# Kernel tuning notes

Hardware: AMD Instinct MI355X
Metric: run time of the kernel (lower is better)

## Reference

```python
import jax, jax.numpy as jnp
import numpy as np
from jax import lax

STRIDE = 4
SCALES = (32.0, 64.0, 128.0)
RATIOS = (0.5, 1.0, 2.0)
PRE_NMS = 6000          # pre_nms_top_n['testing']
POST_NMS = 1000         # post_nms_top_n['testing']
NMS_THRESH = 0.7
MIN_SIZE = 1.0


def make_anchors(fh, fw):
    # 9 base anchors per cell (3 scales x 3 ratios), xyxy centered at cell centers.
    base = []
    for s in SCALES:
        for r in RATIOS:
            w = s * np.sqrt(1.0 / r)
            h = s * np.sqrt(r)
            base.append([-w / 2, -h / 2, w / 2, h / 2])
    base = np.asarray(base, np.float32)                      # [9,4]
    xs = (np.arange(fw, dtype=np.float32) + 0.5) * STRIDE
    ys = (np.arange(fh, dtype=np.float32) + 0.5) * STRIDE
    cx, cy = np.meshgrid(xs, ys)                             # [fh,fw]
    shifts = np.stack([cx, cy, cx, cy], -1)[:, :, None, :]   # [fh,fw,1,4]
    return jnp.asarray((shifts + base[None, None]).reshape(-1, 4))  # [fh*fw*9,4]


def conv(x, w, b):
    y = lax.conv_general_dilated(x, w, (1, 1), 'SAME',
                                 dimension_numbers=('NCHW', 'OIHW', 'NCHW'))
    return y + b[None, :, None, None]


def decode(anchors, deltas):
    wa = anchors[:, 2] - anchors[:, 0]
    ha = anchors[:, 3] - anchors[:, 1]
    cxa = anchors[:, 0] + 0.5 * wa
    cya = anchors[:, 1] + 0.5 * ha
    cx = deltas[:, 0] * wa + cxa
    cy = deltas[:, 1] * ha + cya
    w = jnp.exp(deltas[:, 2]) * wa
    h = jnp.exp(deltas[:, 3]) * ha
    return jnp.stack([cx - 0.5 * w, cy - 0.5 * h, cx + 0.5 * w, cy + 0.5 * h], -1)


def pairwise_iou(a, b):
    area_a = (a[:, 2] - a[:, 0]) * (a[:, 3] - a[:, 1])
    area_b = (b[:, 2] - b[:, 0]) * (b[:, 3] - b[:, 1])
    lt = jnp.maximum(a[:, None, :2], b[None, :, :2])
    rb = jnp.minimum(a[:, None, 2:], b[None, :, 2:])
    wh = jnp.clip(rb - lt, 0.0)
    inter = wh[..., 0] * wh[..., 1]
    return inter / (area_a[:, None] + area_b[None, :] - inter + 1e-9)


def nms_keep(boxes, valid, thresh):
    # boxes already sorted by score descending; greedy suppression.
    n = boxes.shape[0]
    iou = pairwise_iou(boxes, boxes)  # [n,n]
    def body(i, keep):
        suppressed = jnp.any((iou[i] > thresh) & keep)
        return keep.at[i].set(valid[i] & ~suppressed)
    return lax.fori_loop(0, n, body, jnp.zeros(n, bool))


def rpn_forward(feature, w1, b1, w_cls, b_cls, w_reg, b_reg, image_h, image_w,
                detach_for_proposal=True):
    fh, fw = feature.shape[2], feature.shape[3]
    x = jax.nn.relu(conv(feature, w1, b1))
    conf = conv(x, w_cls, b_cls).transpose(0, 2, 3, 1).reshape(-1)        # [N]
    offsets = conv(x, w_reg, b_reg).transpose(0, 2, 3, 1).reshape(-1, 4)  # [N,4]
    if detach_for_proposal:  # original detaches before create_proposal
        conf = lax.stop_gradient(conf)
        offsets = lax.stop_gradient(offsets)
    anchors = make_anchors(fh, fw)

    pre_n = min(PRE_NMS, conf.shape[0])
    scores, idx = lax.top_k(conf, pre_n)
    props = decode(anchors[idx], offsets[idx])
    # process_box: clip to image, drop boxes smaller than min_size (mask form)
    props = jnp.stack([jnp.clip(props[:, 0], 0.0, float(image_w)),
                       jnp.clip(props[:, 1], 0.0, float(image_h)),
                       jnp.clip(props[:, 2], 0.0, float(image_w)),
                       jnp.clip(props[:, 3], 0.0, float(image_h))], -1)
    valid = ((props[:, 2] - props[:, 0]) >= MIN_SIZE) & \
            ((props[:, 3] - props[:, 1]) >= MIN_SIZE)

    keep = nms_keep(lax.stop_gradient(props), valid, NMS_THRESH)
    # compact first POST_NMS kept boxes into a fixed-shape output (zero padded)
    rank = jnp.cumsum(keep) - 1
    dest = jnp.where(keep & (rank < POST_NMS), rank, POST_NMS)
    out = jnp.zeros((POST_NMS + 1, 4), props.dtype).at[dest].set(props)[:POST_NMS]
    return out


def setup_inputs() -> dict:
    key = jax.random.key(0)
    ks = jax.random.split(key, 4)
    return {
        'feature': jax.random.normal(ks[0], (1, 256, 200, 272), jnp.float32),
        'w1': jax.random.normal(ks[1], (256, 256, 3, 3), jnp.float32) * 0.02,
        'b1': jnp.zeros((256,), jnp.float32),
        'w_cls': jax.random.normal(ks[2], (9, 256, 1, 1), jnp.float32) * 0.02,
        'b_cls': jnp.zeros((9,), jnp.float32),
        'w_reg': jax.random.normal(ks[3], (36, 256, 1, 1), jnp.float32) * 0.01,
        'b_reg': jnp.zeros((36,), jnp.float32),
        'image_h': 800,
        'image_w': 1088,
    }


def reference(feature, w1, b1, w_cls, b_cls, w_reg, b_reg, image_h, image_w):
    return rpn_forward(feature, w1, b1, w_cls, b_cls, w_reg, b_reg,
                       image_h, image_w, detach_for_proposal=True)
```

## Files before the change

### kernel.cpp

```cpp
#include <hip/hip_runtime.h>
#include <hip/hip_bf16.h>
#include <math.h>

#define H_ 200
#define W_ 272
#define C_ 256
#define HW 54400
#define NANCH 489600
#define PRE_N 6000
#define POST_N 1000
#define NWORDS 94
#define CHUNK_W 2720

#define X_OFF       0ull
#define CONF_OFF    55705600ull
#define HIST1_OFF   57664000ull
#define HIST2_OFF   57926144ull
#define SCAL_OFF    58188288ull
#define SEL_OFF     58188544ull
#define TOPIDX_OFF  58254080ull
#define BOXES_OFF   58278080ull
#define VALID_OFF   58374080ull
#define MASK_OFF    58398080ull
#define W1R_OFF     62910080ull
#define WCR_OFF     65269376ull

__device__ __forceinline__ unsigned fkey(float fv) {
    unsigned u = __float_as_uint(fv);
    return (u & 0x80000000u) ? ~u : (u | 0x80000000u);
}

__global__ __launch_bounds__(256) void k_init(const float* __restrict__ w1,
                                              const float* __restrict__ wcls,
                                              unsigned* __restrict__ hist1,
                                              float* __restrict__ w1r,
                                              float* __restrict__ wcr) {
    int e = blockIdx.x * 256 + threadIdx.x;
    if (e < 131136) hist1[e] = 0u;
    int e1 = e - 131136;
    if (e1 >= 0 && e1 < 589824) {
        int oc = e1 / 2304; int rem = e1 % 2304; int ic = rem / 9; int k = rem % 9;
        int wg = oc >> 3, o = oc & 7;
        w1r[(((size_t)wg * 256 + ic) * 9 + k) * 8 + o] = w1[e1];
    } else if (e1 >= 589824 && e1 < 589824 + 2304) {
        int e2 = e1 - 589824; int a = e2 / 256; int c = e2 % 256;
        wcr[c * 9 + a] = wcls[e2];
    }
}

__global__ __launch_bounds__(256) void k_conv1(const float* __restrict__ f,
                                               const float* __restrict__ w1r,
                                               const float* __restrict__ b1,
                                               float* __restrict__ xo) {
    __shared__ __align__(16) float sI[2][2880];
    int tid = threadIdx.x;
    int lane = tid & 63;
    int wgl = __builtin_amdgcn_readfirstlane(tid >> 6);
    int xg = lane & 7;
    int yg = lane >> 3;
    int X0 = blockIdx.x * 32;
    int Y0 = blockIdx.y * 8;
    int wg = blockIdx.z * 4 + wgl;
    int y = Y0 + yg;
    int xbase = X0 + xg * 4;

    int off[11]; int lds[11]; bool ok[11];
#pragma unroll
    for (int it = 0; it < 11; it++) {
        int l = tid + it * 256;
        int ci = l / 340; int r = l - ci * 340; int ry = r / 34; int rx = r - ry * 34;
        int gx = X0 - 1 + rx, gy = Y0 - 1 + ry;
        ok[it] = (l < CHUNK_W) && gx >= 0 && gx < W_ && gy >= 0 && gy < H_;
        off[it] = ci * HW + gy * W_ + gx;
        lds[it] = (ci * 10 + ry) * 36 + rx;
    }
    float rbuf[11];
#pragma unroll
    for (int it = 0; it < 11; it++)
        rbuf[it] = ok[it] ? f[off[it]] : 0.f;
#pragma unroll
    for (int it = 0; it < 11; it++)
        if (tid + it * 256 < CHUNK_W) sI[0][lds[it]] = rbuf[it];
    __syncthreads();

    float acc[8][4];
#pragma unroll
    for (int o = 0; o < 8; o++)
#pragma unroll
        for (int i = 0; i < 4; i++) acc[o][i] = 0.f;

    const float* wbase = w1r + (size_t)wg * 256 * 72;

    int cur = 0;
    for (int ic0 = 0; ic0 < 256; ic0 += 8) {
        if (ic0 < 248) {
            const float* fn = f + (size_t)(ic0 + 8) * HW;
#pragma unroll
            for (int it = 0; it < 11; it++)
                rbuf[it] = ok[it] ? fn[off[it]] : 0.f;
        }
        const float* sbuf = sI[cur];
        for (int ci = 0; ci < 8; ci++) {
            const float* wp = wbase + (size_t)(ic0 + ci) * 72;
#pragma unroll
            for (int ky = 0; ky < 3; ky++) {
                const float* irow = &sbuf[(ci * 10 + yg + ky) * 36 + xg * 4];
                float4 va = *(const float4*)irow;
                float2 vb = *(const float2*)(irow + 4);
                float in[6] = {va.x, va.y, va.z, va.w, vb.x, vb.y};
                const float* wrow = wp + ky * 24;
#pragma unroll
                for (int kx = 0; kx < 3; kx++) {
#pragma unroll
                    for (int o = 0; o < 8; o++) {
                        float w = wrow[kx * 8 + o];
#pragma unroll
                        for (int i = 0; i < 4; i++)
                            acc[o][i] = fmaf(w, in[i + kx], acc[o][i]);
                    }
                }
            }
        }
        if (ic0 < 248) {
#pragma unroll
            for (int it = 0; it < 11; it++)
                if (tid + it * 256 < CHUNK_W) sI[cur ^ 1][lds[it]] = rbuf[it];
        }
        __syncthreads();
        cur ^= 1;
    }
#pragma unroll
    for (int o = 0; o < 8; o++) {
        int oc = wg * 8 + o;
        float bv = b1[oc];
        float* orow = xo + (size_t)oc * HW + y * W_ + xbase;
        float v0 = fmaxf(acc[o][0] + bv, 0.f), v1 = fmaxf(acc[o][1] + bv, 0.f);
        float v2 = fmaxf(acc[o][2] + bv, 0.f), v3 = fmaxf(acc[o][3] + bv, 0.f);
        if (xbase + 3 < W_) {
            *(float4*)orow = make_float4(v0, v1, v2, v3);
        } else {
            float vv[4] = {v0, v1, v2, v3};
            for (int i = 0; i < 4; i++)
                if (xbase + i < W_) orow[i] = vv[i];
        }
    }
}

__global__ __launch_bounds__(256) void k_cls(const float* __restrict__ x,
                                             const float* __restrict__ wcr,
                                             const float* __restrict__ bc,
                                             float* __restrict__ conf,
                                             unsigned* __restrict__ hist) {
    int p = blockIdx.x * 256 + threadIdx.x;
    if (p >= HW) return;
    float acc[9];
#pragma unroll
    for (int a = 0; a < 9; a++) acc[a] = 0.f;
    for (int c = 0; c < 256; c++) {
        float xv = x[c * HW + p];
        const float* wp = wcr + c * 9;
#pragma unroll
        for (int a = 0; a < 9; a++) acc[a] = fmaf(wp[a], xv, acc[a]);
    }
#pragma unroll
    for (int a = 0; a < 9; a++) {
        float v = acc[a] + bc[a];
        conf[p * 9 + a] = v;
        atomicAdd(&hist[fkey(v) >> 16], 1u);
    }
}

__global__ __launch_bounds__(256) void k_hist2(const float* __restrict__ conf,
                                               const unsigned* __restrict__ scal, unsigned* hist) {
    int n = blockIdx.x * 256 + threadIdx.x;
    if (n >= NANCH) return;
    unsigned key = fkey(conf[n]);
    if ((key >> 16) == scal[0]) atomicAdd(&hist[key & 0xFFFFu], 1u);
}

__global__ __launch_bounds__(1024) void k_scan(const unsigned* __restrict__ hist,
                                               unsigned* scal, int mode) {
    __shared__ unsigned ssum[1024];
    int t = threadIdx.x;
    unsigned target = 6000u - (mode ? scal[1] : 0u);
    int base = 65535 - t * 64;
    unsigned s = 0;
    for (int k = 0; k < 64; k++) s += hist[base - k];
    ssum[t] = s;
    __syncthreads();
    for (int off = 1; off < 1024; off <<= 1) {
        unsigned v = (t >= off) ? ssum[t - off] : 0u;
        __syncthreads();
        ssum[t] += v;
        __syncthreads();
    }
    unsigned incl = ssum[t], excl = incl - s;
    if (excl < target && target <= incl) {
        unsigned run = excl;
        for (int k = 0; k < 64; k++) {
            unsigned c = hist[base - k];
            if (run + c >= target) { scal[2 * mode] = (unsigned)(base - k); scal[2 * mode + 1] = run; break; }
            run += c;
        }
    }
}

__global__ __launch_bounds__(256) void k_gather(const float* __restrict__ conf,
                                                unsigned* scal, unsigned long long* sel) {
    int n = blockIdx.x * 256 + threadIdx.x;
    if (n >= NANCH) return;
    unsigned B1 = scal[0], cnt1 = scal[1], B2 = scal[2], cnt2 = scal[3];
    unsigned T = (B1 << 16) | B2;
    unsigned key = fkey(conf[n]);
    if (key < T) return;
    unsigned long long kk = ((unsigned long long)(~key) << 32) | (unsigned)n;
    if (key > T) {
        unsigned pos = atomicAdd(&scal[4], 1u);
        if (pos < 8192u) sel[pos] = kk;
    } else {
        unsigned pos = cnt1 + cnt2 + atomicAdd(&scal[5], 1u);
        if (pos < 8192u) sel[pos] = kk;
    }
}

__global__ __launch_bounds__(256) void k_rank(const unsigned* __restrict__ scal,
                                              const unsigned long long* __restrict__ sel,
                                              unsigned* __restrict__ topidx) {
    __shared__ unsigned long long tile[2048];
    unsigned G = scal[1] + scal[3];
    unsigned filled = G + scal[5];
    if (filled > 8192u) filled = 8192u;
    int i = blockIdx.x * 256 + threadIdx.x;
    unsigned long long mykey = (i < (int)filled) ? sel[i] : 0xFFFFFFFFFFFFFFFFull;
    int rank = 0;
    for (int t0 = 0; t0 < 8192; t0 += 2048) {
        __syncthreads();
        for (int l = threadIdx.x; l < 2048; l += 256) {
            int j = t0 + l;
            tile[l] = (j < (int)filled) ? sel[j] : 0xFFFFFFFFFFFFFFFFull;
        }
        __syncthreads();
        for (int l = 0; l < 2048; l += 4) {
            ulonglong2 p = *(const ulonglong2*)&tile[l];
            ulonglong2 q = *(const ulonglong2*)&tile[l + 2];
            rank += (p.x < mykey) + (p.y < mykey) + (q.x < mykey) + (q.y < mykey);
        }
    }
    if (i < (int)filled && rank < PRE_N)
        topidx[rank] = (unsigned)(mykey & 0xFFFFFFFFull);
}

__global__ __launch_bounds__(64) void k_prop(const float* __restrict__ x,
                                             const float* __restrict__ wreg,
                                             const float* __restrict__ breg,
                                             const unsigned* __restrict__ topidx,
                                             const int* __restrict__ imh, const int* __restrict__ imw,
                                             float* __restrict__ boxes, int* __restrict__ valid) {
    int r = blockIdx.x;
    int lane = threadIdx.x;
    unsigned n = topidx[r];
    int a = (int)(n % 9u); int p = (int)(n / 9u);
    const float* wr = wreg + (4 * a) * 256;
    float s0 = 0, s1 = 0, s2 = 0, s3 = 0;
    for (int c = lane; c < 256; c += 64) {
        float xv = x[c * HW + p];
        s0 = fmaf(wr[c], xv, s0);
        s1 = fmaf(wr[256 + c], xv, s1);
        s2 = fmaf(wr[512 + c], xv, s2);
        s3 = fmaf(wr[768 + c], xv, s3);
    }
#pragma unroll
    for (int off = 32; off >= 1; off >>= 1) {
        s0 += __shfl_down(s0, off);
        s1 += __shfl_down(s1, off);
        s2 += __shfl_down(s2, off);
        s3 += __shfl_down(s3, off);
    }
    if (lane == 0) {
        float dx = s0 + breg[4 * a], dy = s1 + breg[4 * a + 1];
        float dw = s2 + breg[4 * a + 2], dh = s3 + breg[4 * a + 3];
        int wi = p % W_, hi = p / W_;
        const double SC[3] = {32.0, 64.0, 128.0};
        const double RT[3] = {0.5, 1.0, 2.0};
        double sd = SC[a / 3], rd = RT[a % 3];
        double wb = sd * sqrt(1.0 / rd), hb = sd * sqrt(rd);
        float bx1 = (float)(-wb * 0.5), by1 = (float)(-hb * 0.5);
        float bx2 = (float)(wb * 0.5),  by2 = (float)(hb * 0.5);
        float cxs = ((float)wi + 0.5f) * 4.0f, cys = ((float)hi + 0.5f) * 4.0f;
        float x1a = cxs + bx1, y1a = cys + by1, x2a = cxs + bx2, y2a = cys + by2;
        float wa = x2a - x1a, ha = y2a - y1a;
        float cxa = x1a + 0.5f * wa, cya = y1a + 0.5f * ha;
        float cx = dx * wa + cxa, cy = dy * ha + cya;
        float ww = expf(dw) * wa, hh = expf(dh) * ha;
        float X1 = cx - 0.5f * ww, Y1 = cy - 0.5f * hh;
        float X2 = cx + 0.5f * ww, Y2 = cy + 0.5f * hh;
        float Wf = (float)(*imw), Hf = (float)(*imh);
        X1 = fminf(fmaxf(X1, 0.f), Wf); Y1 = fminf(fmaxf(Y1, 0.f), Hf);
        X2 = fminf(fmaxf(X2, 0.f), Wf); Y2 = fminf(fmaxf(Y2, 0.f), Hf);
        boxes[4 * r] = X1; boxes[4 * r + 1] = Y1; boxes[4 * r + 2] = X2; boxes[4 * r + 3] = Y2;
        valid[r] = ((X2 - X1) >= 1.0f && (Y2 - Y1) >= 1.0f) ? 1 : 0;
    }
}

__global__ __launch_bounds__(256) void k_mask(const float* __restrict__ boxes,
                                              unsigned long long* __restrict__ mask) {
    __shared__ float jb[256];
    int jw = blockIdx.x;
    int i = blockIdx.y * 256 + threadIdx.x;
    {
        int idx = jw * 256 + threadIdx.x;
        jb[threadIdx.x] = (idx < PRE_N * 4) ? boxes[idx] : 0.f;
    }
    __syncthreads();
    if (i >= PRE_N) return;
    float ax1 = boxes[4 * i], ay1 = boxes[4 * i + 1], ax2 = boxes[4 * i + 2], ay2 = boxes[4 * i + 3];
    float aarea = (ax2 - ax1) * (ay2 - ay1);
    unsigned long long m = 0;
    int jbase = jw * 64;
    for (int b = 0; b < 64; b++) {
        int j = jbase + b;
        if (j <= i || j >= PRE_N) continue;
        float bx1 = jb[4 * b], by1 = jb[4 * b + 1], bx2 = jb[4 * b + 2], by2 = jb[4 * b + 3];
        float barea = (bx2 - bx1) * (by2 - by1);
        float xx1 = fmaxf(ax1, bx1), yy1 = fmaxf(ay1, by1);
        float xx2 = fminf(ax2, bx2), yy2 = fminf(ay2, by2);
        float w = fmaxf(xx2 - xx1, 0.f), h = fmaxf(yy2 - yy1, 0.f);
        float inter = w * h;
        float iou = inter / (aarea + barea - inter + 1e-9f);
        if (iou > 0.7f) m |= (1ull << b);
    }
    mask[(size_t)i * NWORDS + jw] = m;
}

__global__ __launch_bounds__(128) void k_scan_nms(const unsigned long long* __restrict__ mask,
                                                  const int* __restrict__ valid,
                                                  const float* __restrict__ boxes,
                                                  float* __restrict__ out) {
    __shared__ unsigned long long diag[NWORDS][64];
    __shared__ unsigned long long removed[NWORDS];
    __shared__ unsigned long long validw[NWORDS];
    __shared__ int keepList[POST_N];
    __shared__ int cnt;
    __shared__ unsigned long long keptbits;
    int t = threadIdx.x;
    if (t < NWORDS) { removed[t] = 0ull; validw[t] = 0ull; }
    if (t == 0) cnt = 0;
    __syncthreads();
    for (int l = t; l < NWORDS * 64; l += 128) {
        int w = l >> 6, b = l & 63;
        int i = w * 64 + b;
        diag[w][b] = (i < PRE_N) ? mask[(size_t)i * NWORDS + w] : 0ull;
    }
    for (int i = t; i < PRE_N; i += 128)
        if (valid[i]) atomicOr(&validw[i >> 6], 1ull << (i & 63));
    __syncthreads();
    for (int w = 0; w < NWORDS; w++) {
        unsigned long long candw = validw[w] & ~removed[w];
        if (!candw) continue;
        if (t == 0) {
            unsigned long long cand = candw;
            unsigned long long kb = 0ull;
            int c = cnt;
            while (cand && c < POST_N) {
                int b = __ffsll((unsigned long long)cand) - 1;
                keepList[c++] = w * 64 + b;
                kb |= 1ull << b;
                cand &= ~(1ull << b);
                cand &= ~diag[w][b];
            }
            cnt = c; keptbits = kb;
        }
        __syncthreads();
        if (cnt >= POST_N) break;
        unsigned long long kb = keptbits;
        if (kb) {
            for (int w2 = w + 1 + t; w2 < NWORDS; w2 += 128) {
                unsigned long long acc2 = removed[w2];
                unsigned long long tt = kb;
                while (tt) {
                    int b = __ffsll((unsigned long long)tt) - 1;
                    tt &= tt - 1;
                    acc2 |= mask[(size_t)(w * 64 + b) * NWORDS + w2];
                }
                removed[w2] = acc2;
            }
        }
        __syncthreads();
    }
    __syncthreads();
    int c = cnt;
    for (int e = t; e < POST_N * 4; e += 128) {
        int r = e >> 2;
        out[e] = (r < c) ? boxes[4 * keepList[r] + (e & 3)] : 0.f;
    }
}

extern "C" void kernel_launch(void* const* d_in, const int* in_sizes, int n_in,
                              void* d_out, int out_size, void* d_ws, size_t ws_size,
                              hipStream_t stream) {
    const float* feature = (const float*)d_in[0];
    const float* w1   = (const float*)d_in[1];
    const float* b1   = (const float*)d_in[2];
    const float* wcls = (const float*)d_in[3];
    const float* bcls = (const float*)d_in[4];
    const float* wreg = (const float*)d_in[5];
    const float* breg = (const float*)d_in[6];
    const int* imh = (const int*)d_in[7];
    const int* imw = (const int*)d_in[8];

    char* ws = (char*)d_ws;
    float* xbuf  = (float*)(ws + X_OFF);
    float* conf  = (float*)(ws + CONF_OFF);
    unsigned* hist1 = (unsigned*)(ws + HIST1_OFF);
    unsigned* hist2 = (unsigned*)(ws + HIST2_OFF);
    unsigned* scal  = (unsigned*)(ws + SCAL_OFF);
    unsigned long long* sel = (unsigned long long*)(ws + SEL_OFF);
    unsigned* topidx = (unsigned*)(ws + TOPIDX_OFF);
    float* boxes = (float*)(ws + BOXES_OFF);
    int* valid   = (int*)(ws + VALID_OFF);
    unsigned long long* mask = (unsigned long long*)(ws + MASK_OFF);
    float* w1r = (float*)(ws + W1R_OFF);
    float* wcr = (float*)(ws + WCR_OFF);
    float* outF = (float*)d_out;

    hipLaunchKernelGGL(k_init,   dim3(2826), dim3(256), 0, stream, w1, wcls, hist1, w1r, wcr);
    hipLaunchKernelGGL(k_conv1,  dim3(9, 25, 8), dim3(256), 0, stream, feature, w1r, b1, xbuf);
    hipLaunchKernelGGL(k_cls,    dim3(213),  dim3(256), 0, stream, xbuf, wcr, bcls, conf, hist1);
    hipLaunchKernelGGL(k_scan,   dim3(1),    dim3(1024), 0, stream, hist1, scal, 0);
    hipLaunchKernelGGL(k_hist2,  dim3(1913), dim3(256), 0, stream, conf, scal, hist2);
    hipLaunchKernelGGL(k_scan,   dim3(1),    dim3(1024), 0, stream, hist2, scal, 1);
    hipLaunchKernelGGL(k_gather, dim3(1913), dim3(256), 0, stream, conf, scal, sel);
    hipLaunchKernelGGL(k_rank,   dim3(32),   dim3(256), 0, stream, scal, sel, topidx);
    hipLaunchKernelGGL(k_prop,   dim3(PRE_N), dim3(64), 0, stream, xbuf, wreg, breg, topidx, imh, imw, boxes, valid);
    hipLaunchKernelGGL(k_mask,   dim3(NWORDS, 24), dim3(256), 0, stream, boxes, mask);
    hipLaunchKernelGGL(k_scan_nms, dim3(1), dim3(128), 0, stream, mask, valid, boxes, outF);
}
```

Baseline: 1.594 ms.

## Fuse post-conv pipeline into one cooperative persistent kernel with grid syncs

Replaces the nine post-convolution launches (cls head, two histogram/scan passes, gather, rank, proposal decode, IoU mask, NMS scan) with a single cooperative kernel of 256 blocks that separates the stages with grid.sync. The aim is to remove per-launch overhead and idle gaps between the many small serial kernels. In exchange, the wide stages (cls head and the full-anchor passes) now run on only 256 blocks with grid-stride loops, giving less occupancy than before. The single-block scans and NMS also leave the rest of the grid waiting at the barriers.

```diff
diff --git a/kernel.cpp b/kernel.cpp
--- a/kernel.cpp
+++ b/kernel.cpp
@@ -1,6 +1,9 @@
 #include <hip/hip_runtime.h>
 #include <hip/hip_bf16.h>
+#include <hip/hip_cooperative_groups.h>
 #include <math.h>
+
+namespace cg = cooperative_groups;
 
 #define H_ 200
 #define W_ 272
@@ -146,252 +149,299 @@
     }
 }
 
-__global__ __launch_bounds__(256) void k_cls(const float* __restrict__ x,
-                                             const float* __restrict__ wcr,
-                                             const float* __restrict__ bc,
-                                             float* __restrict__ conf,
-                                             unsigned* __restrict__ hist) {
-    int p = blockIdx.x * 256 + threadIdx.x;
-    if (p >= HW) return;
-    float acc[9];
-#pragma unroll
-    for (int a = 0; a < 9; a++) acc[a] = 0.f;
-    for (int c = 0; c < 256; c++) {
-        float xv = x[c * HW + p];
-        const float* wp = wcr + c * 9;
-#pragma unroll
-        for (int a = 0; a < 9; a++) acc[a] = fmaf(wp[a], xv, acc[a]);
-    }
-#pragma unroll
-    for (int a = 0; a < 9; a++) {
-        float v = acc[a] + bc[a];
-        conf[p * 9 + a] = v;
-        atomicAdd(&hist[fkey(v) >> 16], 1u);
-    }
-}
-
-__global__ __launch_bounds__(256) void k_hist2(const float* __restrict__ conf,
-                                               const unsigned* __restrict__ scal, unsigned* hist) {
-    int n = blockIdx.x * 256 + threadIdx.x;
-    if (n >= NANCH) return;
-    unsigned key = fkey(conf[n]);
-    if ((key >> 16) == scal[0]) atomicAdd(&hist[key & 0xFFFFu], 1u);
-}
-
-__global__ __launch_bounds__(1024) void k_scan(const unsigned* __restrict__ hist,
-                                               unsigned* scal, int mode) {
-    __shared__ unsigned ssum[1024];
+union SharedU {
+    unsigned ssum[256];
+    unsigned long long tile[2048];
+    float jb[256];
+    struct {
+        unsigned long long diag[NWORDS][64];
+        unsigned long long removed[NWORDS];
+        unsigned long long validw[NWORDS];
+        int keepList[POST_N];
+        int cnt;
+        unsigned long long keptbits;
+    } nms;
+};
+
+__global__ __launch_bounds__(256) void k_post(const float* __restrict__ x,
+                                              const float* __restrict__ wcr,
+                                              const float* __restrict__ bc,
+                                              float* __restrict__ conf,
+                                              unsigned* __restrict__ hist1,
+                                              unsigned* __restrict__ hist2,
+                                              unsigned* __restrict__ scal,
+                                              unsigned long long* __restrict__ sel,
+                                              unsigned* __restrict__ topidx,
+                                              const float* __restrict__ wreg,
+                                              const float* __restrict__ breg,
+                                              const int* __restrict__ imh,
+                                              const int* __restrict__ imw,
+                                              float* __restrict__ boxes,
+                                              int* __restrict__ validA,
+                                              unsigned long long* __restrict__ mask,
+                                              float* __restrict__ out) {
+    __shared__ SharedU su;
+    cg::grid_group grid = cg::this_grid();
     int t = threadIdx.x;
-    unsigned target = 6000u - (mode ? scal[1] : 0u);
-    int base = 65535 - t * 64;
-    unsigned s = 0;
-    for (int k = 0; k < 64; k++) s += hist[base - k];
-    ssum[t] = s;
-    __syncthreads();
-    for (int off = 1; off < 1024; off <<= 1) {
-        unsigned v = (t >= off) ? ssum[t - off] : 0u;
-        __syncthreads();
-        ssum[t] += v;
-        __syncthreads();
-    }
-    unsigned incl = ssum[t], excl = incl - s;
-    if (excl < target && target <= incl) {
-        unsigned run = excl;
-        for (int k = 0; k < 64; k++) {
-            unsigned c = hist[base - k];
-            if (run + c >= target) { scal[2 * mode] = (unsigned)(base - k); scal[2 * mode + 1] = run; break; }
-            run += c;
-        }
-    }
-}
-
-__global__ __launch_bounds__(256) void k_gather(const float* __restrict__ conf,
-                                                unsigned* scal, unsigned long long* sel) {
-    int n = blockIdx.x * 256 + threadIdx.x;
-    if (n >= NANCH) return;
-    unsigned B1 = scal[0], cnt1 = scal[1], B2 = scal[2], cnt2 = scal[3];
-    unsigned T = (B1 << 16) | B2;
-    unsigned key = fkey(conf[n]);
-    if (key < T) return;
-    unsigned long long kk = ((unsigned long long)(~key) << 32) | (unsigned)n;
-    if (key > T) {
-        unsigned pos = atomicAdd(&scal[4], 1u);
-        if (pos < 8192u) sel[pos] = kk;
-    } else {
-        unsigned pos = cnt1 + cnt2 + atomicAdd(&scal[5], 1u);
-        if (pos < 8192u) sel[pos] = kk;
-    }
-}
-
-__global__ __launch_bounds__(256) void k_rank(const unsigned* __restrict__ scal,
-                                              const unsigned long long* __restrict__ sel,
-                                              unsigned* __restrict__ topidx) {
-    __shared__ unsigned long long tile[2048];
-    unsigned G = scal[1] + scal[3];
-    unsigned filled = G + scal[5];
-    if (filled > 8192u) filled = 8192u;
-    int i = blockIdx.x * 256 + threadIdx.x;
-    unsigned long long mykey = (i < (int)filled) ? sel[i] : 0xFFFFFFFFFFFFFFFFull;
-    int rank = 0;
-    for (int t0 = 0; t0 < 8192; t0 += 2048) {
-        __syncthreads();
-        for (int l = threadIdx.x; l < 2048; l += 256) {
-            int j = t0 + l;
-            tile[l] = (j < (int)filled) ? sel[j] : 0xFFFFFFFFFFFFFFFFull;
-        }
-        __syncthreads();
-        for (int l = 0; l < 2048; l += 4) {
-            ulonglong2 p = *(const ulonglong2*)&tile[l];
-            ulonglong2 q = *(const ulonglong2*)&tile[l + 2];
-            rank += (p.x < mykey) + (p.y < mykey) + (q.x < mykey) + (q.y < mykey);
-        }
-    }
-    if (i < (int)filled && rank < PRE_N)
-        topidx[rank] = (unsigned)(mykey & 0xFFFFFFFFull);
-}
-
-__global__ __launch_bounds__(64) void k_prop(const float* __restrict__ x,
-                                             const float* __restrict__ wreg,
-                                             const float* __restrict__ breg,
-                                             const unsigned* __restrict__ topidx,
-                                             const int* __restrict__ imh, const int* __restrict__ imw,
-                                             float* __restrict__ boxes, int* __restrict__ valid) {
-    int r = blockIdx.x;
-    int lane = threadIdx.x;
-    unsigned n = topidx[r];
-    int a = (int)(n % 9u); int p = (int)(n / 9u);
-    const float* wr = wreg + (4 * a) * 256;
-    float s0 = 0, s1 = 0, s2 = 0, s3 = 0;
-    for (int c = lane; c < 256; c += 64) {
-        float xv = x[c * HW + p];
-        s0 = fmaf(wr[c], xv, s0);
-        s1 = fmaf(wr[256 + c], xv, s1);
-        s2 = fmaf(wr[512 + c], xv, s2);
-        s3 = fmaf(wr[768 + c], xv, s3);
-    }
-#pragma unroll
-    for (int off = 32; off >= 1; off >>= 1) {
-        s0 += __shfl_down(s0, off);
-        s1 += __shfl_down(s1, off);
-        s2 += __shfl_down(s2, off);
-        s3 += __shfl_down(s3, off);
-    }
-    if (lane == 0) {
-        float dx = s0 + breg[4 * a], dy = s1 + breg[4 * a + 1];
-        float dw = s2 + breg[4 * a + 2], dh = s3 + breg[4 * a + 3];
-        int wi = p % W_, hi = p / W_;
-        const double SC[3] = {32.0, 64.0, 128.0};
-        const double RT[3] = {0.5, 1.0, 2.0};
-        double sd = SC[a / 3], rd = RT[a % 3];
-        double wb = sd * sqrt(1.0 / rd), hb = sd * sqrt(rd);
-        float bx1 = (float)(-wb * 0.5), by1 = (float)(-hb * 0.5);
-        float bx2 = (float)(wb * 0.5),  by2 = (float)(hb * 0.5);
-        float cxs = ((float)wi + 0.5f) * 4.0f, cys = ((float)hi + 0.5f) * 4.0f;
-        float x1a = cxs + bx1, y1a = cys + by1, x2a = cxs + bx2, y2a = cys + by2;
-        float wa = x2a - x1a, ha = y2a - y1a;
-        float cxa = x1a + 0.5f * wa, cya = y1a + 0.5f * ha;
-        float cx = dx * wa + cxa, cy = dy * ha + cya;
-        float ww = expf(dw) * wa, hh = expf(dh) * ha;
-        float X1 = cx - 0.5f * ww, Y1 = cy - 0.5f * hh;
-        float X2 = cx + 0.5f * ww, Y2 = cy + 0.5f * hh;
-        float Wf = (float)(*imw), Hf = (float)(*imh);
-        X1 = fminf(fmaxf(X1, 0.f), Wf); Y1 = fminf(fmaxf(Y1, 0.f), Hf);
-        X2 = fminf(fmaxf(X2, 0.f), Wf); Y2 = fminf(fmaxf(Y2, 0.f), Hf);
-        boxes[4 * r] = X1; boxes[4 * r + 1] = Y1; boxes[4 * r + 2] = X2; boxes[4 * r + 3] = Y2;
-        valid[r] = ((X2 - X1) >= 1.0f && (Y2 - Y1) >= 1.0f) ? 1 : 0;
-    }
-}
-
-__global__ __launch_bounds__(256) void k_mask(const float* __restrict__ boxes,
-                                              unsigned long long* __restrict__ mask) {
-    __shared__ float jb[256];
-    int jw = blockIdx.x;
-    int i = blockIdx.y * 256 + threadIdx.x;
+    int gid = blockIdx.x * 256 + t;
+
+    for (int p = gid; p < HW; p += 65536) {
+        float acc[9];
+#pragma unroll
+        for (int a = 0; a < 9; a++) acc[a] = 0.f;
+        for (int c = 0; c < 256; c++) {
+            float xv = x[c * HW + p];
+            const float* wp = wcr + c * 9;
+#pragma unroll
+            for (int a = 0; a < 9; a++) acc[a] = fmaf(wp[a], xv, acc[a]);
+        }
+#pragma unroll
+        for (int a = 0; a < 9; a++) {
+            float v = acc[a] + bc[a];
+            conf[p * 9 + a] = v;
+            atomicAdd(&hist1[fkey(v) >> 16], 1u);
+        }
+    }
+    grid.sync();
+
+    if (blockIdx.x == 0) {
+        unsigned target = 6000u;
+        int base = 65535 - t * 256;
+        unsigned s = 0;
+        const uint4* hp = (const uint4*)(hist1 + (base - 255));
+        for (int k = 0; k < 64; k++) { uint4 v = hp[k]; s += v.x + v.y + v.z + v.w; }
+        su.ssum[t] = s;
+        __syncthreads();
+        for (int o = 1; o < 256; o <<= 1) {
+            unsigned v = (t >= o) ? su.ssum[t - o] : 0u;
+            __syncthreads();
+            su.ssum[t] += v;
+            __syncthreads();
+        }
+        unsigned incl = su.ssum[t], excl = incl - s;
+        if (excl < target && target <= incl) {
+            unsigned run = excl;
+            for (int k = 0; k < 256; k++) {
+                unsigned c = hist1[base - k];
+                if (run + c >= target) { scal[0] = (unsigned)(base - k); scal[1] = run; break; }
+                run += c;
+            }
+        }
+    }
+    grid.sync();
+
     {
-        int idx = jw * 256 + threadIdx.x;
-        jb[threadIdx.x] = (idx < PRE_N * 4) ? boxes[idx] : 0.f;
-    }
-    __syncthreads();
-    if (i >= PRE_N) return;
-    float ax1 = boxes[4 * i], ay1 = boxes[4 * i + 1], ax2 = boxes[4 * i + 2], ay2 = boxes[4 * i + 3];
-    float aarea = (ax2 - ax1) * (ay2 - ay1);
-    unsigned long long m = 0;
-    int jbase = jw * 64;
-    for (int b = 0; b < 64; b++) {
-        int j = jbase + b;
-        if (j <= i || j >= PRE_N) continue;
-        float bx1 = jb[4 * b], by1 = jb[4 * b + 1], bx2 = jb[4 * b + 2], by2 = jb[4 * b + 3];
-        float barea = (bx2 - bx1) * (by2 - by1);
-        float xx1 = fmaxf(ax1, bx1), yy1 = fmaxf(ay1, by1);
-        float xx2 = fminf(ax2, bx2), yy2 = fminf(ay2, by2);
-        float w = fmaxf(xx2 - xx1, 0.f), h = fmaxf(yy2 - yy1, 0.f);
-        float inter = w * h;
-        float iou = inter / (aarea + barea - inter + 1e-9f);
-        if (iou > 0.7f) m |= (1ull << b);
-    }
-    mask[(size_t)i * NWORDS + jw] = m;
-}
-
-__global__ __launch_bounds__(128) void k_scan_nms(const unsigned long long* __restrict__ mask,
-                                                  const int* __restrict__ valid,
-                                                  const float* __restrict__ boxes,
-                                                  float* __restrict__ out) {
-    __shared__ unsigned long long diag[NWORDS][64];
-    __shared__ unsigned long long removed[NWORDS];
-    __shared__ unsigned long long validw[NWORDS];
-    __shared__ int keepList[POST_N];
-    __shared__ int cnt;
-    __shared__ unsigned long long keptbits;
-    int t = threadIdx.x;
-    if (t < NWORDS) { removed[t] = 0ull; validw[t] = 0ull; }
-    if (t == 0) cnt = 0;
-    __syncthreads();
-    for (int l = t; l < NWORDS * 64; l += 128) {
-        int w = l >> 6, b = l & 63;
-        int i = w * 64 + b;
-        diag[w][b] = (i < PRE_N) ? mask[(size_t)i * NWORDS + w] : 0ull;
-    }
-    for (int i = t; i < PRE_N; i += 128)
-        if (valid[i]) atomicOr(&validw[i >> 6], 1ull << (i & 63));
-    __syncthreads();
-    for (int w = 0; w < NWORDS; w++) {
-        unsigned long long candw = validw[w] & ~removed[w];
-        if (!candw) continue;
-        if (t == 0) {
-            unsigned long long cand = candw;
-            unsigned long long kb = 0ull;
-            int c = cnt;
-            while (cand && c < POST_N) {
-                int b = __ffsll((unsigned long long)cand) - 1;
-                keepList[c++] = w * 64 + b;
-                kb |= 1ull << b;
-                cand &= ~(1ull << b);
-                cand &= ~diag[w][b];
-            }
-            cnt = c; keptbits = kb;
-        }
-        __syncthreads();
-        if (cnt >= POST_N) break;
-        unsigned long long kb = keptbits;
-        if (kb) {
-            for (int w2 = w + 1 + t; w2 < NWORDS; w2 += 128) {
-                unsigned long long acc2 = removed[w2];
-                unsigned long long tt = kb;
-                while (tt) {
-                    int b = __ffsll((unsigned long long)tt) - 1;
-                    tt &= tt - 1;
-                    acc2 |= mask[(size_t)(w * 64 + b) * NWORDS + w2];
+        unsigned B1 = scal[0];
+        for (int n = gid; n < NANCH; n += 65536) {
+            unsigned key = fkey(conf[n]);
+            if ((key >> 16) == B1) atomicAdd(&hist2[key & 0xFFFFu], 1u);
+        }
+    }
+    grid.sync();
+
+    if (blockIdx.x == 0) {
+        unsigned target = 6000u - scal[1];
+        int base = 65535 - t * 256;
+        unsigned s = 0;
+        const uint4* hp = (const uint4*)(hist2 + (base - 255));
+        for (int k = 0; k < 64; k++) { uint4 v = hp[k]; s += v.x + v.y + v.z + v.w; }
+        su.ssum[t] = s;
+        __syncthreads();
+        for (int o = 1; o < 256; o <<= 1) {
+            unsigned v = (t >= o) ? su.ssum[t - o] : 0u;
+            __syncthreads();
+            su.ssum[t] += v;
+            __syncthreads();
+        }
+        unsigned incl = su.ssum[t], excl = incl - s;
+        if (excl < target && target <= incl) {
+            unsigned run = excl;
+            for (int k = 0; k < 256; k++) {
+                unsigned c = hist2[base - k];
+                if (run + c >= target) { scal[2] = (unsigned)(base - k); scal[3] = run; break; }
+                run += c;
+            }
+        }
+    }
+    grid.sync();
+
+    {
+        unsigned B1 = scal[0], cnt1 = scal[1], B2 = scal[2], cnt2 = scal[3];
+        unsigned T = (B1 << 16) | B2;
+        for (int n = gid; n < NANCH; n += 65536) {
+            unsigned key = fkey(conf[n]);
+            if (key < T) continue;
+            unsigned long long kk = ((unsigned long long)(~key) << 32) | (unsigned)n;
+            if (key > T) {
+                unsigned pos = atomicAdd(&scal[4], 1u);
+                if (pos < 8192u) sel[pos] = kk;
+            } else {
+                unsigned pos = cnt1 + cnt2 + atomicAdd(&scal[5], 1u);
+                if (pos < 8192u) sel[pos] = kk;
+            }
+        }
+    }
+    grid.sync();
+
+    {
+        unsigned G = scal[1] + scal[3];
+        unsigned filled = G + scal[5];
+        if (filled > 8192u) filled = 8192u;
+        if (blockIdx.x < 32) {
+            int i = blockIdx.x * 256 + t;
+            unsigned long long mykey = (i < (int)filled) ? sel[i] : 0xFFFFFFFFFFFFFFFFull;
+            int rank = 0;
+            for (int t0 = 0; t0 < 8192; t0 += 2048) {
+                __syncthreads();
+                for (int l = t; l < 2048; l += 256) {
+                    int j = t0 + l;
+                    su.tile[l] = (j < (int)filled) ? sel[j] : 0xFFFFFFFFFFFFFFFFull;
                 }
-                removed[w2] = acc2;
-            }
-        }
-        __syncthreads();
-    }
-    __syncthreads();
-    int c = cnt;
-    for (int e = t; e < POST_N * 4; e += 128) {
-        int r = e >> 2;
-        out[e] = (r < c) ? boxes[4 * keepList[r] + (e & 3)] : 0.f;
+                __syncthreads();
+                for (int l = 0; l < 2048; l += 4) {
+                    ulonglong2 p = *(const ulonglong2*)&su.tile[l];
+                    ulonglong2 q = *(const ulonglong2*)&su.tile[l + 2];
+                    rank += (p.x < mykey) + (p.y < mykey) + (q.x < mykey) + (q.y < mykey);
+                }
+            }
+            if (i < (int)filled && rank < PRE_N)
+                topidx[rank] = (unsigned)(mykey & 0xFFFFFFFFull);
+        }
+    }
+    grid.sync();
+
+    {
+        int wave = blockIdx.x * 4 + (t >> 6);
+        int lane = t & 63;
+        for (int r = wave; r < PRE_N; r += 1024) {
+            unsigned n = topidx[r];
+            int a = (int)(n % 9u); int p = (int)(n / 9u);
+            const float* wr = wreg + (4 * a) * 256;
+            float s0 = 0, s1 = 0, s2 = 0, s3 = 0;
+            for (int c = lane; c < 256; c += 64) {
+                float xv = x[c * HW + p];
+                s0 = fmaf(wr[c], xv, s0);
+                s1 = fmaf(wr[256 + c], xv, s1);
+                s2 = fmaf(wr[512 + c], xv, s2);
+                s3 = fmaf(wr[768 + c], xv, s3);
+            }
+#pragma unroll
+            for (int o = 32; o >= 1; o >>= 1) {
+                s0 += __shfl_down(s0, o);
+                s1 += __shfl_down(s1, o);
+                s2 += __shfl_down(s2, o);
+                s3 += __shfl_down(s3, o);
+            }
+            if (lane == 0) {
+                float dx = s0 + breg[4 * a], dy = s1 + breg[4 * a + 1];
+                float dw = s2 + breg[4 * a + 2], dh = s3 + breg[4 * a + 3];
+                int wi = p % W_, hi = p / W_;
+                const double SC[3] = {32.0, 64.0, 128.0};
+                const double RT[3] = {0.5, 1.0, 2.0};
+                double sd = SC[a / 3], rd = RT[a % 3];
+                double wb = sd * sqrt(1.0 / rd), hb = sd * sqrt(rd);
+                float bx1 = (float)(-wb * 0.5), by1 = (float)(-hb * 0.5);
+                float bx2 = (float)(wb * 0.5),  by2 = (float)(hb * 0.5);
+                float cxs = ((float)wi + 0.5f) * 4.0f, cys = ((float)hi + 0.5f) * 4.0f;
+                float x1a = cxs + bx1, y1a = cys + by1, x2a = cxs + bx2, y2a = cys + by2;
+                float wa = x2a - x1a, ha = y2a - y1a;
+                float cxa = x1a + 0.5f * wa, cya = y1a + 0.5f * ha;
+                float cx = dx * wa + cxa, cy = dy * ha + cya;
+                float ww = expf(dw) * wa, hh = expf(dh) * ha;
+                float X1 = cx - 0.5f * ww, Y1 = cy - 0.5f * hh;
+                float X2 = cx + 0.5f * ww, Y2 = cy + 0.5f * hh;
+                float Wf = (float)(*imw), Hf = (float)(*imh);
+                X1 = fminf(fmaxf(X1, 0.f), Wf); Y1 = fminf(fmaxf(Y1, 0.f), Hf);
+                X2 = fminf(fmaxf(X2, 0.f), Wf); Y2 = fminf(fmaxf(Y2, 0.f), Hf);
+                boxes[4 * r] = X1; boxes[4 * r + 1] = Y1; boxes[4 * r + 2] = X2; boxes[4 * r + 3] = Y2;
+                validA[r] = ((X2 - X1) >= 1.0f && (Y2 - Y1) >= 1.0f) ? 1 : 0;
+            }
+        }
+    }
+    grid.sync();
+
+    for (int tile = blockIdx.x; tile < NWORDS * 24; tile += 256) {
+        int jw = tile / 24, ib = tile - jw * 24;
+        __syncthreads();
+        {
+            int idx = jw * 256 + t;
+            su.jb[t] = (idx < PRE_N * 4) ? boxes[idx] : 0.f;
+        }
+        __syncthreads();
+        int i = ib * 256 + t;
+        if (i < PRE_N) {
+            float ax1 = boxes[4 * i], ay1 = boxes[4 * i + 1], ax2 = boxes[4 * i + 2], ay2 = boxes[4 * i + 3];
+            float aarea = (ax2 - ax1) * (ay2 - ay1);
+            unsigned long long m = 0;
+            int jbase = jw * 64;
+            for (int b = 0; b < 64; b++) {
+                int j = jbase + b;
+                if (j <= i || j >= PRE_N) continue;
+                float bx1 = su.jb[4 * b], by1 = su.jb[4 * b + 1], bx2 = su.jb[4 * b + 2], by2 = su.jb[4 * b + 3];
+                float barea = (bx2 - bx1) * (by2 - by1);
+                float xx1 = fmaxf(ax1, bx1), yy1 = fmaxf(ay1, by1);
+                float xx2 = fminf(ax2, bx2), yy2 = fminf(ay2, by2);
+                float w = fmaxf(xx2 - xx1, 0.f), h = fmaxf(yy2 - yy1, 0.f);
+                float inter = w * h;
+                float iou = inter / (aarea + barea - inter + 1e-9f);
+                if (iou > 0.7f) m |= (1ull << b);
+            }
+            mask[(size_t)i * NWORDS + jw] = m;
+        }
+    }
+    grid.sync();
+
+    if (blockIdx.x == 0) {
+        if (t < NWORDS) { su.nms.removed[t] = 0ull; su.nms.validw[t] = 0ull; }
+        if (t == 0) su.nms.cnt = 0;
+        __syncthreads();
+        for (int l = t; l < NWORDS * 64; l += 256) {
+            int w = l >> 6, b = l & 63;
+            int i = w * 64 + b;
+            su.nms.diag[w][b] = (i < PRE_N) ? mask[(size_t)i * NWORDS + w] : 0ull;
+        }
+        for (int i = t; i < PRE_N; i += 256)
+            if (validA[i]) atomicOr(&su.nms.validw[i >> 6], 1ull << (i & 63));
+        __syncthreads();
+        for (int w = 0; w < NWORDS; w++) {
+            unsigned long long candw = su.nms.validw[w] & ~su.nms.removed[w];
+            if (!candw) continue;
+            if (t == 0) {
+                unsigned long long cand = candw;
+                unsigned long long kb = 0ull;
+                int c = su.nms.cnt;
+                while (cand && c < POST_N) {
+                    int b = __ffsll((unsigned long long)cand) - 1;
+                    su.nms.keepList[c++] = w * 64 + b;
+                    kb |= 1ull << b;
+                    cand &= ~(1ull << b);
+                    cand &= ~su.nms.diag[w][b];
+                }
+                su.nms.cnt = c; su.nms.keptbits = kb;
+            }
+            __syncthreads();
+            if (su.nms.cnt >= POST_N) break;
+            unsigned long long kb = su.nms.keptbits;
+            if (kb) {
+                for (int w2 = w + 1 + t; w2 < NWORDS; w2 += 256) {
+                    unsigned long long acc2 = su.nms.removed[w2];
+                    unsigned long long tt = kb;
+                    while (tt) {
+                        int b = __ffsll((unsigned long long)tt) - 1;
+                        tt &= tt - 1;
+                        acc2 |= mask[(size_t)(w * 64 + b) * NWORDS + w2];
+                    }
+                    su.nms.removed[w2] = acc2;
+                }
+            }
+            __syncthreads();
+        }
+        __syncthreads();
+        int c = su.nms.cnt;
+        for (int e = t; e < POST_N * 4; e += 256) {
+            int r = e >> 2;
+            out[e] = (r < c) ? boxes[4 * su.nms.keepList[r] + (e & 3)] : 0.f;
+        }
     }
 }
 
@@ -423,15 +473,13 @@
     float* wcr = (float*)(ws + WCR_OFF);
     float* outF = (float*)d_out;
 
-    hipLaunchKernelGGL(k_init,   dim3(2826), dim3(256), 0, stream, w1, wcls, hist1, w1r, wcr);
-    hipLaunchKernelGGL(k_conv1,  dim3(9, 25, 8), dim3(256), 0, stream, feature, w1r, b1, xbuf);
-    hipLaunchKernelGGL(k_cls,    dim3(213),  dim3(256), 0, stream, xbuf, wcr, bcls, conf, hist1);
-    hipLaunchKernelGGL(k_scan,   dim3(1),    dim3(1024), 0, stream, hist1, scal, 0);
-    hipLaunchKernelGGL(k_hist2,  dim3(1913), dim3(256), 0, stream, conf, scal, hist2);
-    hipLaunchKernelGGL(k_scan,   dim3(1),    dim3(1024), 0, stream, hist2, scal, 1);
-    hipLaunchKernelGGL(k_gather, dim3(1913), dim3(256), 0, stream, conf, scal, sel);
-    hipLaunchKernelGGL(k_rank,   dim3(32),   dim3(256), 0, stream, scal, sel, topidx);
-    hipLaunchKernelGGL(k_prop,   dim3(PRE_N), dim3(64), 0, stream, xbuf, wreg, breg, topidx, imh, imw, boxes, valid);
-    hipLaunchKernelGGL(k_mask,   dim3(NWORDS, 24), dim3(256), 0, stream, boxes, mask);
-    hipLaunchKernelGGL(k_scan_nms, dim3(1), dim3(128), 0, stream, mask, valid, boxes, outF);
+    hipLaunchKernelGGL(k_init,  dim3(2826), dim3(256), 0, stream, w1, wcls, hist1, w1r, wcr);
+    hipLaunchKernelGGL(k_conv1, dim3(9, 25, 8), dim3(256), 0, stream, feature, w1r, b1, xbuf);
+
+    void* args[] = {(void*)&xbuf, (void*)&wcr, (void*)&bcls, (void*)&conf,
+                    (void*)&hist1, (void*)&hist2, (void*)&scal, (void*)&sel,
+                    (void*)&topidx, (void*)&wreg, (void*)&breg, (void*)&imh,
+                    (void*)&imw, (void*)&boxes, (void*)&valid, (void*)&mask,
+                    (void*)&outF};
+    hipLaunchCooperativeKernel((void*)k_post, dim3(256), dim3(256), args, 0, stream);
 }
```

New measurement: 1.826 ms. 14.6% more time.

## Fold init into conv, drop second histogram pass, and use single-level radix select

Applied to the files above, without the earlier changes.

Removes the separate init kernel. Zeroing of the histogram, scalars and selection buffer, plus the cls-weight transpose, now happen at the start of the conv kernel. The conv kernel reads the original OIHW weights directly instead of a pre-transposed copy. The two-level radix select becomes one level: candidates in the threshold bucket go into a larger selection buffer and are ranked by brute-force compare, with early exit past the filled count. This removes a launch, the second histogram pass and a scan. The trade-offs are more scattered scalar weight loads inside the conv inner loop and more rank work when the tie bucket is large. Selection may be wrong if the tie bucket overflows the buffer capacity.

```diff
diff --git a/kernel.cpp b/kernel.cpp
--- a/kernel.cpp
+++ b/kernel.cpp
@@ -11,18 +11,17 @@
 #define POST_N 1000
 #define NWORDS 94
 #define CHUNK_W 2720
+#define SELCAP 16384
 
 #define X_OFF       0ull
 #define CONF_OFF    55705600ull
 #define HIST1_OFF   57664000ull
-#define HIST2_OFF   57926144ull
+#define SEL_OFF     57926144ull
 #define SCAL_OFF    58188288ull
-#define SEL_OFF     58188544ull
 #define TOPIDX_OFF  58254080ull
 #define BOXES_OFF   58278080ull
 #define VALID_OFF   58374080ull
 #define MASK_OFF    58398080ull
-#define W1R_OFF     62910080ull
 #define WCR_OFF     65269376ull
 
 __device__ __forceinline__ unsigned fkey(float fv) {
@@ -30,30 +29,30 @@
     return (u & 0x80000000u) ? ~u : (u | 0x80000000u);
 }
 
-__global__ __launch_bounds__(256) void k_init(const float* __restrict__ w1,
-                                              const float* __restrict__ wcls,
-                                              unsigned* __restrict__ hist1,
-                                              float* __restrict__ w1r,
-                                              float* __restrict__ wcr) {
-    int e = blockIdx.x * 256 + threadIdx.x;
-    if (e < 131136) hist1[e] = 0u;
-    int e1 = e - 131136;
-    if (e1 >= 0 && e1 < 589824) {
-        int oc = e1 / 2304; int rem = e1 % 2304; int ic = rem / 9; int k = rem % 9;
-        int wg = oc >> 3, o = oc & 7;
-        w1r[(((size_t)wg * 256 + ic) * 9 + k) * 8 + o] = w1[e1];
-    } else if (e1 >= 589824 && e1 < 589824 + 2304) {
-        int e2 = e1 - 589824; int a = e2 / 256; int c = e2 % 256;
-        wcr[c * 9 + a] = wcls[e2];
-    }
-}
-
 __global__ __launch_bounds__(256) void k_conv1(const float* __restrict__ f,
-                                               const float* __restrict__ w1r,
+                                               const float* __restrict__ w1,
                                                const float* __restrict__ b1,
-                                               float* __restrict__ xo) {
+                                               float* __restrict__ xo,
+                                               unsigned* __restrict__ hist1,
+                                               unsigned* __restrict__ scal,
+                                               unsigned long long* __restrict__ sel,
+                                               const float* __restrict__ wcls,
+                                               float* __restrict__ wcr) {
     __shared__ __align__(16) float sI[2][2880];
     int tid = threadIdx.x;
+    int fb = blockIdx.x + 9 * (blockIdx.y + 25 * blockIdx.z);
+    {
+        int g = fb * 256 + tid;
+        if (g < 65536) hist1[g] = 0u;
+        else if (g < 65600) scal[g - 65536] = 0u;
+        else if (g < 98368) ((unsigned*)sel)[g - 65600] = 0xFFFFFFFFu;
+    }
+    if (fb == 0) {
+        for (int e = tid; e < 2304; e += 256) {
+            int a = e / 256, c = e % 256;
+            wcr[c * 9 + a] = wcls[e];
+        }
+    }
     int lane = tid & 63;
     int wgl = __builtin_amdgcn_readfirstlane(tid >> 6);
     int xg = lane & 7;
@@ -89,7 +88,7 @@
 #pragma unroll
         for (int i = 0; i < 4; i++) acc[o][i] = 0.f;
 
-    const float* wbase = w1r + (size_t)wg * 256 * 72;
+    const float* wbase = w1 + (size_t)(wg * 8) * 2304;
 
     int cur = 0;
     for (int ic0 = 0; ic0 < 256; ic0 += 8) {
@@ -101,19 +100,18 @@
         }
         const float* sbuf = sI[cur];
         for (int ci = 0; ci < 8; ci++) {
-            const float* wp = wbase + (size_t)(ic0 + ci) * 72;
+            const float* wci = wbase + (ic0 + ci) * 9;
 #pragma unroll
             for (int ky = 0; ky < 3; ky++) {
                 const float* irow = &sbuf[(ci * 10 + yg + ky) * 36 + xg * 4];
                 float4 va = *(const float4*)irow;
                 float2 vb = *(const float2*)(irow + 4);
                 float in[6] = {va.x, va.y, va.z, va.w, vb.x, vb.y};
-                const float* wrow = wp + ky * 24;
 #pragma unroll
                 for (int kx = 0; kx < 3; kx++) {
 #pragma unroll
                     for (int o = 0; o < 8; o++) {
-                        float w = wrow[kx * 8 + o];
+                        float w = wci[o * 2304 + ky * 3 + kx];
 #pragma unroll
                         for (int i = 0; i < 4; i++)
                             acc[o][i] = fmaf(w, in[i + kx], acc[o][i]);
@@ -170,22 +168,17 @@
     }
 }
 
-__global__ __launch_bounds__(256) void k_hist2(const float* __restrict__ conf,
-                                               const unsigned* __restrict__ scal, unsigned* hist) {
-    int n = blockIdx.x * 256 + threadIdx.x;
-    if (n >= NANCH) return;
-    unsigned key = fkey(conf[n]);
-    if ((key >> 16) == scal[0]) atomicAdd(&hist[key & 0xFFFFu], 1u);
-}
-
 __global__ __launch_bounds__(1024) void k_scan(const unsigned* __restrict__ hist,
-                                               unsigned* scal, int mode) {
+                                               unsigned* scal) {
     __shared__ unsigned ssum[1024];
     int t = threadIdx.x;
-    unsigned target = 6000u - (mode ? scal[1] : 0u);
     int base = 65535 - t * 64;
     unsigned s = 0;
-    for (int k = 0; k < 64; k++) s += hist[base - k];
+    {
+        const uint4* hp = (const uint4*)(hist + (base - 63));
+#pragma unroll
+        for (int k = 0; k < 16; k++) { uint4 v = hp[k]; s += v.x + v.y + v.z + v.w; }
+    }
     ssum[t] = s;
     __syncthreads();
     for (int off = 1; off < 1024; off <<= 1) {
@@ -195,12 +188,22 @@
         __syncthreads();
     }
     unsigned incl = ssum[t], excl = incl - s;
-    if (excl < target && target <= incl) {
+    if (excl < 6000u && 6000u <= incl) {
         unsigned run = excl;
-        for (int k = 0; k < 64; k++) {
-            unsigned c = hist[base - k];
-            if (run + c >= target) { scal[2 * mode] = (unsigned)(base - k); scal[2 * mode + 1] = run; break; }
-            run += c;
+        bool found = false;
+        for (int pass = 0; pass < 2 && !found; pass++) {
+            unsigned c32[32];
+#pragma unroll
+            for (int j = 0; j < 32; j++) c32[j] = hist[base - (pass * 32 + j)];
+            for (int j = 0; j < 32; j++) {
+                if (run + c32[j] >= 6000u) {
+                    scal[0] = (unsigned)(base - (pass * 32 + j));
+                    scal[1] = run;
+                    found = true;
+                    break;
+                }
+                run += c32[j];
+            }
         }
     }
 }
@@ -209,17 +212,17 @@
                                                 unsigned* scal, unsigned long long* sel) {
     int n = blockIdx.x * 256 + threadIdx.x;
     if (n >= NANCH) return;
-    unsigned B1 = scal[0], cnt1 = scal[1], B2 = scal[2], cnt2 = scal[3];
-    unsigned T = (B1 << 16) | B2;
+    unsigned B1 = scal[0], cnt1 = scal[1];
     unsigned key = fkey(conf[n]);
-    if (key < T) return;
+    unsigned pre = key >> 16;
+    if (pre < B1) return;
     unsigned long long kk = ((unsigned long long)(~key) << 32) | (unsigned)n;
-    if (key > T) {
+    if (pre > B1) {
         unsigned pos = atomicAdd(&scal[4], 1u);
-        if (pos < 8192u) sel[pos] = kk;
+        sel[pos] = kk;
     } else {
-        unsigned pos = cnt1 + cnt2 + atomicAdd(&scal[5], 1u);
-        if (pos < 8192u) sel[pos] = kk;
+        unsigned pos = cnt1 + atomicAdd(&scal[5], 1u);
+        if (pos < SELCAP) sel[pos] = kk;
     }
 }
 
@@ -227,18 +230,16 @@
                                               const unsigned long long* __restrict__ sel,
                                               unsigned* __restrict__ topidx) {
     __shared__ unsigned long long tile[2048];
-    unsigned G = scal[1] + scal[3];
-    unsigned filled = G + scal[5];
-    if (filled > 8192u) filled = 8192u;
+    unsigned filled = scal[1] + scal[5];
+    if (filled > SELCAP) filled = SELCAP;
     int i = blockIdx.x * 256 + threadIdx.x;
-    unsigned long long mykey = (i < (int)filled) ? sel[i] : 0xFFFFFFFFFFFFFFFFull;
+    unsigned long long mykey = sel[i];
     int rank = 0;
-    for (int t0 = 0; t0 < 8192; t0 += 2048) {
-        __syncthreads();
-        for (int l = threadIdx.x; l < 2048; l += 256) {
-            int j = t0 + l;
-            tile[l] = (j < (int)filled) ? sel[j] : 0xFFFFFFFFFFFFFFFFull;
-        }
+    for (int t0 = 0; t0 < SELCAP; t0 += 2048) {
+        if (t0 >= (int)filled) break;
+        __syncthreads();
+        for (int l = threadIdx.x; l < 2048; l += 256)
+            tile[l] = sel[t0 + l];
         __syncthreads();
         for (int l = 0; l < 2048; l += 4) {
             ulonglong2 p = *(const ulonglong2*)&tile[l];
@@ -412,25 +413,21 @@
     float* xbuf  = (float*)(ws + X_OFF);
     float* conf  = (float*)(ws + CONF_OFF);
     unsigned* hist1 = (unsigned*)(ws + HIST1_OFF);
-    unsigned* hist2 = (unsigned*)(ws + HIST2_OFF);
     unsigned* scal  = (unsigned*)(ws + SCAL_OFF);
     unsigned long long* sel = (unsigned long long*)(ws + SEL_OFF);
     unsigned* topidx = (unsigned*)(ws + TOPIDX_OFF);
     float* boxes = (float*)(ws + BOXES_OFF);
     int* valid   = (int*)(ws + VALID_OFF);
     unsigned long long* mask = (unsigned long long*)(ws + MASK_OFF);
-    float* w1r = (float*)(ws + W1R_OFF);
     float* wcr = (float*)(ws + WCR_OFF);
     float* outF = (float*)d_out;
 
-    hipLaunchKernelGGL(k_init,   dim3(2826), dim3(256), 0, stream, w1, wcls, hist1, w1r, wcr);
-    hipLaunchKernelGGL(k_conv1,  dim3(9, 25, 8), dim3(256), 0, stream, feature, w1r, b1, xbuf);
+    hipLaunchKernelGGL(k_conv1,  dim3(9, 25, 8), dim3(256), 0, stream,
+                       feature, w1, b1, xbuf, hist1, scal, sel, wcls, wcr);
     hipLaunchKernelGGL(k_cls,    dim3(213),  dim3(256), 0, stream, xbuf, wcr, bcls, conf, hist1);
-    hipLaunchKernelGGL(k_scan,   dim3(1),    dim3(1024), 0, stream, hist1, scal, 0);
-    hipLaunchKernelGGL(k_hist2,  dim3(1913), dim3(256), 0, stream, conf, scal, hist2);
-    hipLaunchKernelGGL(k_scan,   dim3(1),    dim3(1024), 0, stream, hist2, scal, 1);
+    hipLaunchKernelGGL(k_scan,   dim3(1),    dim3(1024), 0, stream, hist1, scal);
     hipLaunchKernelGGL(k_gather, dim3(1913), dim3(256), 0, stream, conf, scal, sel);
-    hipLaunchKernelGGL(k_rank,   dim3(32),   dim3(256), 0, stream, scal, sel, topidx);
+    hipLaunchKernelGGL(k_rank,   dim3(64),   dim3(256), 0, stream, scal, sel, topidx);
     hipLaunchKernelGGL(k_prop,   dim3(PRE_N), dim3(64), 0, stream, xbuf, wreg, breg, topidx, imh, imw, boxes, valid);
     hipLaunchKernelGGL(k_mask,   dim3(NWORDS, 24), dim3(256), 0, stream, boxes, mask);
     hipLaunchKernelGGL(k_scan_nms, dim3(1), dim3(128), 0, stream, mask, valid, boxes, outF);
```

New measurement: 1.554 ms. -2.5%, faster.
